# Optimization experiments

Measured on AMD Instinct MI355X. Metric: run time of the kernel, lower is better.

The kernel has to match this reference:

```python
import jax, jax.numpy as jnp
import numpy as np

EPS = 1e-6
T_MAX = 0.999  # occlusion threshold used by compute_paths


def _dot(a, b):
    return jnp.sum(a * b, axis=-1)


def _mirror(p, v, n):
    # Reflect point p across plane through v with unit normal n.
    return p - 2.0 * _dot(p - v, n)[..., None] * n


def image_method(frm, to, mirror_v, mirror_n):
    """frm/to: [...,3]; mirror_v/mirror_n: [...,order,3] -> paths [...,order,3]."""
    order = mirror_v.shape[-2]
    images = []
    cur = frm
    for i in range(order):  # forward pass: successive images of TX
        cur = _mirror(cur, mirror_v[..., i, :], mirror_n[..., i, :])
        images.append(cur)
    paths = [None] * order
    nxt = to
    for i in range(order - 1, -1, -1):  # backward pass: intersect with planes
        img = images[i]
        v = mirror_v[..., i, :]
        n = mirror_n[..., i, :]
        d = nxt - img
        denom = _dot(d, n)
        t = _dot(v - img, n) / jnp.where(jnp.abs(denom) < EPS, EPS, denom)
        nxt = img + t[..., None] * d
        paths[i] = nxt
    return jnp.stack(paths, axis=-2)


def triangles_contain(tv, p):
    """tv: [...,3,3] triangle vertices, p: [...,3] point in same plane -> bool."""
    v0, v1, v2 = tv[..., 0, :], tv[..., 1, :], tv[..., 2, :]
    n0 = jnp.cross(p - v0, v1 - v0)
    n1 = jnp.cross(p - v1, v2 - v1)
    n2 = jnp.cross(p - v2, v0 - v2)
    d01, d12, d20 = _dot(n0, n1), _dot(n1, n2), _dot(n2, n0)
    pos = (d01 >= 0) & (d12 >= 0) & (d20 >= 0)
    neg = (d01 <= 0) & (d12 <= 0) & (d20 <= 0)
    return pos | neg


def same_side_of_mirrors(full_paths, mirror_v, mirror_n):
    """full_paths: [...,order+2,3]; consecutive vertices around each mirror on same side."""
    order = mirror_v.shape[-2]
    prev_v = full_paths[..., :order, :]
    next_v = full_paths[..., 2:, :]
    d_prev = _dot(prev_v - mirror_v, mirror_n)
    d_next = _dot(next_v - mirror_v, mirror_n)
    return d_prev * d_next >= 0


def rays_intersect_triangles(o, d, tv):
    """Moller-Trumbore. o,d: [...,3]; tv: broadcastable [...,3,3] -> (t, hit)."""
    v0, v1, v2 = tv[..., 0, :], tv[..., 1, :], tv[..., 2, :]
    e1 = v1 - v0
    e2 = v2 - v0
    h = jnp.cross(d, e2)
    a = _dot(e1, h)
    inv = 1.0 / jnp.where(jnp.abs(a) < EPS, 1.0, a)
    s = o - v0
    u = _dot(s, h) * inv
    q = jnp.cross(s, e1)
    v = _dot(d, q) * inv
    t = _dot(e2, q) * inv
    hit = (jnp.abs(a) > EPS) & (u >= 0.0) & (v >= 0.0) & (u + v <= 1.0) & (t > EPS)
    return t, hit


def compute_paths(transmitters, receivers, vertices, normals, triangles, path_candidates):
    P = path_candidates.shape[0]
    ntx = transmitters.shape[0]
    nrx = receivers.shape[0]
    all_tv = vertices[triangles]  # [T,3,3]

    frm = jnp.broadcast_to(transmitters[None, :, None, :], (P, ntx, nrx, 3))
    to = jnp.broadcast_to(receivers[None, None, :, :], (P, ntx, nrx, 3))

    pc_tv = all_tv[path_candidates]          # [P,order,3,3]
    mirror_v = pc_tv[..., 0, :]              # [P,order,3]
    mirror_n = normals[path_candidates]      # [P,order,3]
    tvb = pc_tv[:, None, None]               # [P,1,1,order,3,3]
    mvb = mirror_v[:, None, None]            # [P,1,1,order,3]
    mnb = mirror_n[:, None, None]

    paths = image_method(frm, to, mvb, mnb)  # [P,ntx,nrx,order,3]
    mask = jnp.all(triangles_contain(tvb, paths), axis=-1)

    full_paths = jnp.concatenate(
        (frm[..., None, :], paths, to[..., None, :]), axis=-2
    )  # [P,ntx,nrx,order+2,3]
    mask = mask & jnp.all(same_side_of_mirrors(full_paths, mvb, mnb), axis=-1)

    # Occlusion test: each of the order+1 segments vs every mesh triangle.
    ray_o = full_paths[..., :-1, None, :]       # [P,ntx,nrx,order+1,1,3]
    ray_d = jnp.diff(full_paths, axis=-2)[..., None, :]
    t, hit = rays_intersect_triangles(ray_o, ray_d, all_tv)  # [P,ntx,nrx,order+1,T]
    intersect = jnp.any((t < T_MAX) & hit, axis=(-1, -2))
    mask = mask & ~intersect

    # jit-friendly masking (original uses boolean fancy-indexing): zero-out invalid paths.
    return jnp.where(mask[..., None, None], full_paths, 0.0)


def setup_inputs() -> dict:
    key = jax.random.key(0)
    k1, k2, k3, k4 = jax.random.split(key, 4)
    V, T = 100, 128
    transmitters = 5.0 * jax.random.normal(k1, (1, 3), jnp.float32)
    receivers = 5.0 * jax.random.normal(k2, (1, 3), jnp.float32)
    vertices = jax.random.uniform(k3, (V, 3), jnp.float32, -10.0, 10.0)
    triangles = jax.random.randint(k4, (T, 3), 0, V, jnp.int32)
    tv = vertices[triangles]
    n = jnp.cross(tv[:, 1] - tv[:, 0], tv[:, 2] - tv[:, 0])
    normals = n / (jnp.linalg.norm(n, axis=-1, keepdims=True) + 1e-8)
    # generate_all_path_candidates(T, order=2): all ordered pairs (i,j), i != j
    idx = np.arange(T)
    ii, jj = np.meshgrid(idx, idx, indexing="ij")
    m = ii != jj
    path_candidates = jnp.asarray(np.stack([ii[m], jj[m]], axis=-1), jnp.int32)
    return {
        "transmitters": transmitters,
        "receivers": receivers,
        "vertices": vertices,
        "normals": normals,
        "triangles": triangles,
        "path_candidates": path_candidates,
        "order": 2,
    }


def reference(transmitters, receivers, vertices, normals, triangles, path_candidates, order):
    del order  # encoded in path_candidates.shape[-1]
    return compute_paths(transmitters, receivers, vertices, normals, triangles, path_candidates)
```

## Files before the change

kernel.cpp:

```cpp
#include <hip/hip_runtime.h>
#include <hip/hip_bf16.h>

#define EPS_F  1e-6f
#define TMAX_F 0.999f

struct F3 { float x, y, z; };

__device__ __forceinline__ F3 operator-(F3 a, F3 b){ return {a.x-b.x, a.y-b.y, a.z-b.z}; }
__device__ __forceinline__ F3 operator+(F3 a, F3 b){ return {a.x+b.x, a.y+b.y, a.z+b.z}; }
__device__ __forceinline__ F3 operator*(float s, F3 a){ return {s*a.x, s*a.y, s*a.z}; }
__device__ __forceinline__ float dot3(F3 a, F3 b){ return a.x*b.x + a.y*b.y + a.z*b.z; }
__device__ __forceinline__ F3 cross3(F3 a, F3 b){
  return { a.y*b.z - a.z*b.y, a.z*b.x - a.x*b.z, a.x*b.y - a.y*b.x };
}
__device__ __forceinline__ F3 ld3(const float* p){ return {p[0], p[1], p[2]}; }

__device__ __forceinline__ F3 mirror3(F3 p, F3 v, F3 n){
  float d = dot3(p - v, n);
  return p - (2.0f * d) * n;
}

__device__ __forceinline__ F3 plane_pt(F3 img, F3 v, F3 n, F3 nxt){
  F3 d = nxt - img;
  float den = dot3(d, n);
  float sd = (fabsf(den) < EPS_F) ? EPS_F : den;
  float t = dot3(v - img, n) / sd;
  return img + t * d;
}

__device__ __forceinline__ bool tri_contains(F3 a, F3 b, F3 c, F3 p){
  F3 n0 = cross3(p - a, b - a);
  F3 n1 = cross3(p - b, c - b);
  F3 n2 = cross3(p - c, a - c);
  float d01 = dot3(n0, n1), d12 = dot3(n1, n2), d20 = dot3(n2, n0);
  bool pos = (d01 >= 0.f) & (d12 >= 0.f) & (d20 >= 0.f);
  bool neg = (d01 <= 0.f) & (d12 <= 0.f) & (d20 <= 0.f);
  return pos | neg;
}

__device__ __forceinline__ bool mt_block(F3 o, F3 d, F3 a, F3 b, F3 c){
  F3 e1 = b - a, e2 = c - a;
  F3 h = cross3(d, e2);
  float det = dot3(e1, h);
  float safep = (fabsf(det) < EPS_F) ? 1.0f : det;
  float inv = 1.0f / safep;
  F3 s = o - a;
  float u = dot3(s, h) * inv;
  F3 q = cross3(s, e1);
  float v = dot3(d, q) * inv;
  float t = dot3(e2, q) * inv;
  bool hit = (fabsf(det) > EPS_F) & (u >= 0.f) & (v >= 0.f) & (u + v <= 1.f) & (t > EPS_F);
  return hit & (t < TMAX_F);
}

__global__ void __launch_bounds__(256)
paths_kernel(const float* __restrict__ txs, const float* __restrict__ rxs,
             const float* __restrict__ vertices, const float* __restrict__ normals,
             const int* __restrict__ triangles, const int* __restrict__ pc,
             int ntx, int nrx, int total, int T, float* __restrict__ out)
{
  extern __shared__ float smem[];
  float* tvS = smem;
  float* nS  = tvS + T * 9;
  float* fpS = nS + T * 3;
  unsigned int* maskS = reinterpret_cast<unsigned int*>(fpS + 64 * 12);
  unsigned int* occlS = maskS + 2;

  const int tid  = threadIdx.x;
  const int lane = tid & 63;
  const int wid  = tid >> 6;

  const int cbase = blockIdx.x * 64;

  if (wid == 1) occlS[lane] = 0u;

  if (wid == 0) {
    const int c = cbase + lane;
    const bool valid = c < total;
    const int cc = valid ? c : 0;

    const int txrx = ntx * nrx;
    int p, tx, rx;
    if (txrx == 1) { p = cc; tx = 0; rx = 0; }
    else {
      p = cc / txrx;
      const int r = cc - p * txrx;
      tx = r / nrx;
      rx = r - tx * nrx;
    }

    const F3 frm = ld3(txs + tx * 3);
    const F3 to  = ld3(rxs + rx * 3);

    const int2 t01 = reinterpret_cast<const int2*>(pc)[p];
    const int t0 = t01.x, t1 = t01.y;

    const F3 a0 = ld3(vertices + triangles[t0*3+0]*3);
    const F3 b0 = ld3(vertices + triangles[t0*3+1]*3);
    const F3 c0 = ld3(vertices + triangles[t0*3+2]*3);
    const F3 a1 = ld3(vertices + triangles[t1*3+0]*3);
    const F3 b1 = ld3(vertices + triangles[t1*3+1]*3);
    const F3 c1 = ld3(vertices + triangles[t1*3+2]*3);
    const F3 n0 = ld3(normals + t0 * 3);
    const F3 n1 = ld3(normals + t1 * 3);
    const F3 v0 = a0;
    const F3 v1 = a1;

    const F3 img0 = mirror3(frm,  v0, n0);
    const F3 img1 = mirror3(img0, v1, n1);
    const F3 p1 = plane_pt(img1, v1, n1, to);
    const F3 p0 = plane_pt(img0, v0, n0, p1);

    bool mask = tri_contains(a0, b0, c0, p0) & tri_contains(a1, b1, c1, p1);
    float sp0 = dot3(frm - v0, n0) * dot3(p1 - v0, n0);
    float sp1 = dot3(p0  - v1, n1) * dot3(to - v1, n1);
    mask = mask & (sp0 >= 0.f) & (sp1 >= 0.f) & valid;

    float* myfp = fpS + lane * 12;
    myfp[0]=frm.x; myfp[1]=frm.y; myfp[2]=frm.z;
    myfp[3]=p0.x;  myfp[4]=p0.y;  myfp[5]=p0.z;
    myfp[6]=p1.x;  myfp[7]=p1.y;  myfp[8]=p1.z;
    myfp[9]=to.x;  myfp[10]=to.y; myfp[11]=to.z;

    unsigned long long m = __ballot(mask);
    if (lane == 0) {
      maskS[0] = (unsigned int)(m & 0xffffffffu);
      maskS[1] = (unsigned int)(m >> 32);
    }
  }
  __syncthreads();

  const unsigned int m0 = maskS[0], m1 = maskS[1];

  if (m0 | m1) {
    for (int i = tid; i < T * 3; i += 256) {
      int vi = triangles[i];
      tvS[i*3+0] = vertices[vi*3+0];
      tvS[i*3+1] = vertices[vi*3+1];
      tvS[i*3+2] = vertices[vi*3+2];
      nS[i] = normals[i];
    }
    __syncthreads();

    unsigned long long alive = ((unsigned long long)m1 << 32) | m0;
    int item = 0;
    while (alive) {
      const int s = __builtin_ctzll(alive);
      alive &= alive - 1;
      const float* sfp = fpS + s * 12;
      #pragma unroll
      for (int seg = 0; seg < 3; ++seg, ++item) {
        if ((item & 3) != wid) continue;
        F3 o = ld3(sfp + seg * 3);
        F3 e = ld3(sfp + seg * 3 + 3);
        F3 d = e - o;
        bool inter = false;
        for (int t = lane; t < T; t += 64) {
          F3 ta = ld3(tvS + t*9), tb = ld3(tvS + t*9 + 3), tc = ld3(tvS + t*9 + 6);
          inter |= mt_block(o, d, ta, tb, tc);
        }
        unsigned long long hb = __ballot(inter);
        if (lane == 0 && hb) occlS[s] = 1u;
      }
    }
    __syncthreads();
  }

  if (tid < 192) {
    const int cand = tid / 3;
    const int quad = tid - cand * 3;
    const int c = cbase + cand;
    if (c < total) {
      const unsigned int mw = (cand < 32) ? m0 : m1;
      const bool fin = ((mw >> (cand & 31)) & 1u) && !occlS[cand];
      const float* fp = fpS + cand * 12 + quad * 4;
      float4 val = fin ? make_float4(fp[0], fp[1], fp[2], fp[3])
                       : make_float4(0.f, 0.f, 0.f, 0.f);
      reinterpret_cast<float4*>(out)[(size_t)c * 3 + quad] = val;
    }
  }
}

extern "C" void kernel_launch(void* const* d_in, const int* in_sizes, int n_in,
                              void* d_out, int out_size, void* d_ws, size_t ws_size,
                              hipStream_t stream) {
  const float* txs       = (const float*)d_in[0];
  const float* rxs       = (const float*)d_in[1];
  const float* vertices  = (const float*)d_in[2];
  const float* normals   = (const float*)d_in[3];
  const int*   triangles = (const int*)d_in[4];
  const int*   pc        = (const int*)d_in[5];

  const int ntx = in_sizes[0] / 3;
  const int nrx = in_sizes[1] / 3;
  const int T   = in_sizes[4] / 3;
  const int P   = in_sizes[5] / 2;

  float* out = (float*)d_out;

  const long long total = (long long)P * ntx * nrx;
  const int grid = (int)((total + 63) / 64);
  const size_t shmem = (size_t)(T * 12 + 64 * 12 + 2 + 64) * sizeof(float);

  paths_kernel<<<grid, 256, shmem, stream>>>(
      txs, rxs, vertices, normals, triangles, pc, ntx, nrx, (int)total, T, out);
}
```

Baseline: 69.78 us.

## Drop shared triangle staging, test all segments per triangle with early exit

Blocks no longer copy every triangle's vertices and normals into shared memory. Occlusion tests now read them straight from global memory or cache, and each wave checks all three segments of one candidate against each triangle, stopping once any lane finds a hit. Output is zero-filled up front and only surviving candidates write their path, which removes the final staged write pass. The cost is redundant gathered global loads per surviving candidate, plus a second write of the zeroed region.

```diff
diff --git a/kernel.cpp b/kernel.cpp
--- a/kernel.cpp
+++ b/kernel.cpp
@@ -60,19 +60,24 @@
              int ntx, int nrx, int total, int T, float* __restrict__ out)
 {
   extern __shared__ float smem[];
-  float* tvS = smem;
-  float* nS  = tvS + T * 9;
-  float* fpS = nS + T * 3;
+  float* fpS = smem;
   unsigned int* maskS = reinterpret_cast<unsigned int*>(fpS + 64 * 12);
   unsigned int* occlS = maskS + 2;
 
   const int tid  = threadIdx.x;
   const int lane = tid & 63;
   const int wid  = tid >> 6;
-
   const int cbase = blockIdx.x * 64;
 
+  if (tid < 192) {
+    const long long q = (long long)cbase * 3 + tid;
+    if (q < (long long)total * 3)
+      reinterpret_cast<float4*>(out)[q] = make_float4(0.f, 0.f, 0.f, 0.f);
+  }
   if (wid == 1) occlS[lane] = 0u;
+
+  bool mask = false;
+  F3 frm, to, p0, p1;
 
   if (wid == 0) {
     const int c = cbase + lane;
@@ -89,8 +94,8 @@
       rx = r - tx * nrx;
     }
 
-    const F3 frm = ld3(txs + tx * 3);
-    const F3 to  = ld3(rxs + rx * 3);
+    frm = ld3(txs + tx * 3);
+    to  = ld3(rxs + rx * 3);
 
     const int2 t01 = reinterpret_cast<const int2*>(pc)[p];
     const int t0 = t01.x, t1 = t01.y;
@@ -108,19 +113,21 @@
 
     const F3 img0 = mirror3(frm,  v0, n0);
     const F3 img1 = mirror3(img0, v1, n1);
-    const F3 p1 = plane_pt(img1, v1, n1, to);
-    const F3 p0 = plane_pt(img0, v0, n0, p1);
-
-    bool mask = tri_contains(a0, b0, c0, p0) & tri_contains(a1, b1, c1, p1);
+    p1 = plane_pt(img1, v1, n1, to);
+    p0 = plane_pt(img0, v0, n0, p1);
+
+    mask = tri_contains(a0, b0, c0, p0) & tri_contains(a1, b1, c1, p1);
     float sp0 = dot3(frm - v0, n0) * dot3(p1 - v0, n0);
     float sp1 = dot3(p0  - v1, n1) * dot3(to - v1, n1);
     mask = mask & (sp0 >= 0.f) & (sp1 >= 0.f) & valid;
 
-    float* myfp = fpS + lane * 12;
-    myfp[0]=frm.x; myfp[1]=frm.y; myfp[2]=frm.z;
-    myfp[3]=p0.x;  myfp[4]=p0.y;  myfp[5]=p0.z;
-    myfp[6]=p1.x;  myfp[7]=p1.y;  myfp[8]=p1.z;
-    myfp[9]=to.x;  myfp[10]=to.y; myfp[11]=to.z;
+    if (mask) {
+      float* myfp = fpS + lane * 12;
+      myfp[0]=frm.x; myfp[1]=frm.y; myfp[2]=frm.z;
+      myfp[3]=p0.x;  myfp[4]=p0.y;  myfp[5]=p0.z;
+      myfp[6]=p1.x;  myfp[7]=p1.y;  myfp[8]=p1.z;
+      myfp[9]=to.x;  myfp[10]=to.y; myfp[11]=to.z;
+    }
 
     unsigned long long m = __ballot(mask);
     if (lane == 0) {
@@ -133,50 +140,40 @@
   const unsigned int m0 = maskS[0], m1 = maskS[1];
 
   if (m0 | m1) {
-    for (int i = tid; i < T * 3; i += 256) {
-      int vi = triangles[i];
-      tvS[i*3+0] = vertices[vi*3+0];
-      tvS[i*3+1] = vertices[vi*3+1];
-      tvS[i*3+2] = vertices[vi*3+2];
-      nS[i] = normals[i];
-    }
-    __syncthreads();
-
     unsigned long long alive = ((unsigned long long)m1 << 32) | m0;
-    int item = 0;
+    int rank = 0;
     while (alive) {
       const int s = __builtin_ctzll(alive);
       alive &= alive - 1;
-      const float* sfp = fpS + s * 12;
-      #pragma unroll
-      for (int seg = 0; seg < 3; ++seg, ++item) {
-        if ((item & 3) != wid) continue;
-        F3 o = ld3(sfp + seg * 3);
-        F3 e = ld3(sfp + seg * 3 + 3);
-        F3 d = e - o;
+      if ((rank++ & 3) == wid) {
+        const float* sfp = fpS + s * 12;
+        const F3 f0 = ld3(sfp), f1 = ld3(sfp+3), f2 = ld3(sfp+6), f3 = ld3(sfp+9);
+        const F3 d0 = f1 - f0, d1 = f2 - f1, d2 = f3 - f2;
         bool inter = false;
-        for (int t = lane; t < T; t += 64) {
-          F3 ta = ld3(tvS + t*9), tb = ld3(tvS + t*9 + 3), tc = ld3(tvS + t*9 + 6);
-          inter |= mt_block(o, d, ta, tb, tc);
+        for (int base = 0; base < T; base += 64) {
+          const int t = base + lane;
+          if (t < T) {
+            const F3 ta = ld3(vertices + triangles[t*3+0]*3);
+            const F3 tb = ld3(vertices + triangles[t*3+1]*3);
+            const F3 tc = ld3(vertices + triangles[t*3+2]*3);
+            inter |= mt_block(f0, d0, ta, tb, tc);
+            inter |= mt_block(f1, d1, ta, tb, tc);
+            inter |= mt_block(f2, d2, ta, tb, tc);
+          }
+          if (__ballot(inter)) break;
         }
-        unsigned long long hb = __ballot(inter);
+        const unsigned long long hb = __ballot(inter);
         if (lane == 0 && hb) occlS[s] = 1u;
       }
     }
     __syncthreads();
-  }
-
-  if (tid < 192) {
-    const int cand = tid / 3;
-    const int quad = tid - cand * 3;
-    const int c = cbase + cand;
-    if (c < total) {
-      const unsigned int mw = (cand < 32) ? m0 : m1;
-      const bool fin = ((mw >> (cand & 31)) & 1u) && !occlS[cand];
-      const float* fp = fpS + cand * 12 + quad * 4;
-      float4 val = fin ? make_float4(fp[0], fp[1], fp[2], fp[3])
-                       : make_float4(0.f, 0.f, 0.f, 0.f);
-      reinterpret_cast<float4*>(out)[(size_t)c * 3 + quad] = val;
+
+    if (wid == 0 && mask && !occlS[lane]) {
+      const int c = cbase + lane;
+      float4* o4 = reinterpret_cast<float4*>(out + (size_t)c * 12);
+      o4[0] = make_float4(frm.x, frm.y, frm.z, p0.x);
+      o4[1] = make_float4(p0.y,  p0.z,  p1.x,  p1.y);
+      o4[2] = make_float4(p1.z,  to.x,  to.y,  to.z);
     }
   }
 }
@@ -200,7 +197,7 @@
 
   const long long total = (long long)P * ntx * nrx;
   const int grid = (int)((total + 63) / 64);
-  const size_t shmem = (size_t)(T * 12 + 64 * 12 + 2 + 64) * sizeof(float);
+  const size_t shmem = (size_t)(64 * 12 + 2 + 64) * sizeof(float);
 
   paths_kernel<<<grid, 256, shmem, stream>>>(
       txs, rxs, vertices, normals, triangles, pc, ntx, nrx, (int)total, T, out);
```

Measured after the change: 68.24 us. 2.2% less time.
